# Optimization experiments

Measured on AMD Instinct MI355X. Metric: run time of the kernel, lower is better.

The kernel has to match this reference:

```python
import jax, jax.numpy as jnp
import numpy as np
from jax import lax

# LRN hyperparameters (from module __init__)
K = 2.0
KERNEL = 5
ALPHA = 1e-4
BETA = 0.75
PAD = KERNEL // 2


def setup_inputs() -> dict:
    key = jax.random.key(0)
    x = jax.random.normal(key, (16, 96, 224, 224), dtype=jnp.float32)
    return {"x": x}


def reference(x) -> jnp.ndarray:
    # Spatial local response norm: per-channel k x k box sum of squares
    # (equivalent to Unfold(kernel, pad=kernel//2) -> view -> square -> sum over window).
    sq = x * x
    ssq = lax.reduce_window(
        sq,
        jnp.float32(0.0),
        lax.add,
        window_dimensions=(1, 1, KERNEL, KERNEL),
        window_strides=(1, 1, 1, 1),
        padding=((0, 0), (0, 0), (PAD, PAD), (PAD, PAD)),
    )
    denom = (K + ALPHA * ssq) ** BETA
    return x / denom
```

## Files before the change

kernel.cpp:

```cpp
#include <hip/hip_runtime.h>


#define LRN_H 224
#define LRN_W 224
#define LRN_WQ 56
#define LRN_STRIPS 8
#define LRN_ROWS 28
#define LRN_PLANE (LRN_H * LRN_W)

__device__ __forceinline__ float4 lrn_zero4() { return make_float4(0.f, 0.f, 0.f, 0.f); }

__device__ __forceinline__ float4 lrn_rowsum(const float* __restrict__ px, int row, int col, int q) {
    if (row < 0 || row >= LRN_H) return lrn_zero4();
    const float* rp = px + row * LRN_W + col;
    float4 xc = *(const float4*)rp;
    float4 xl = (q > 0)          ? *(const float4*)(rp - 4) : lrn_zero4();
    float4 xr = (q < LRN_WQ - 1) ? *(const float4*)(rp + 4) : lrn_zero4();
    float a  = xl.z * xl.z;
    float b  = xl.w * xl.w;
    float c0 = xc.x * xc.x;
    float c1 = xc.y * xc.y;
    float c2 = xc.z * xc.z;
    float c3 = xc.w * xc.w;
    float d0 = xr.x * xr.x;
    float d1 = xr.y * xr.y;
    float t = c1 + c2;
    float4 r;
    r.x = a + b + c0 + t;
    r.y = b + c0 + t + c3;
    r.z = c0 + t + c3 + d0;
    r.w = t + c3 + d0 + d1;
    return r;
}

__global__ __launch_bounds__(256) void LocalResponseNorm_17420387352942_kernel(
        const float* __restrict__ x, float* __restrict__ out) {
    const int q = threadIdx.x;
    if (q >= LRN_WQ) return;
    const int job = blockIdx.x * 4 + threadIdx.y;
    const int plane = job >> 3;
    const int strip = job & 7;
    const float* px = x + (size_t)plane * LRN_PLANE;
    float* po = out + (size_t)plane * LRN_PLANE;
    const int s0 = strip * LRN_ROWS;
    const int col = q << 2;

    float4 r0 = lrn_rowsum(px, s0 - 2, col, q);
    float4 r1 = lrn_rowsum(px, s0 - 1, col, q);
    float4 r2 = lrn_rowsum(px, s0,     col, q);
    float4 r3 = lrn_rowsum(px, s0 + 1, col, q);

#pragma unroll
    for (int h = s0; h < s0 + LRN_ROWS; ++h) {
        float4 r4 = lrn_rowsum(px, h + 2, col, q);
        float4 s;
        s.x = r0.x + r1.x + r2.x + r3.x + r4.x;
        s.y = r0.y + r1.y + r2.y + r3.y + r4.y;
        s.z = r0.z + r1.z + r2.z + r3.z + r4.z;
        s.w = r0.w + r1.w + r2.w + r3.w + r4.w;

        float4 xv = *(const float4*)(px + h * LRN_W + col);
        float4 o;
        {
            float d = fmaf(1e-4f, s.x, 2.0f);
            float r = __builtin_amdgcn_rsqf(d);
            o.x = xv.x * r * __builtin_amdgcn_sqrtf(r);
        }
        {
            float d = fmaf(1e-4f, s.y, 2.0f);
            float r = __builtin_amdgcn_rsqf(d);
            o.y = xv.y * r * __builtin_amdgcn_sqrtf(r);
        }
        {
            float d = fmaf(1e-4f, s.z, 2.0f);
            float r = __builtin_amdgcn_rsqf(d);
            o.z = xv.z * r * __builtin_amdgcn_sqrtf(r);
        }
        {
            float d = fmaf(1e-4f, s.w, 2.0f);
            float r = __builtin_amdgcn_rsqf(d);
            o.w = xv.w * r * __builtin_amdgcn_sqrtf(r);
        }
        *(float4*)(po + h * LRN_W + col) = o;

        r0 = r1; r1 = r2; r2 = r3; r3 = r4;
    }
}

extern "C" void kernel_launch(void* const* d_in, const int* in_sizes, int n_in,
                              void* d_out, int out_size, void* d_ws, size_t ws_size,
                              hipStream_t stream) {
    const float* x = (const float*)d_in[0];
    float* out = (float*)d_out;
    dim3 block(64, 4, 1);
    dim3 grid(12288 / 4, 1, 1);
    LocalResponseNorm_17420387352942_kernel<<<grid, block, 0, stream>>>(x, out);
}
```

Before: 527.0 us.

## Pack threads densely, prefetch next row, reuse center loads, nontemporal stores

Threads are now packed densely, so no lanes idle (before, 8 of every 64 lanes exited). Strips are taller (56 rows), which cuts halo re-reads. Border handling uses clamped addresses and multiply masks instead of branches. Each row is loaded one iteration ahead for prefetch, and center values are kept in registers rather than re-read for the output. Stores are nontemporal and occupancy is hinted at 6 blocks. The cost is higher register pressure and fewer, longer-running jobs, which may reduce parallelism.

```diff
diff --git a/kernel.cpp b/kernel.cpp
--- a/kernel.cpp
+++ b/kernel.cpp
@@ -1,89 +1,115 @@
 #include <hip/hip_runtime.h>
 
+
+typedef float f4 __attribute__((ext_vector_type(4)));
 
 #define LRN_H 224
 #define LRN_W 224
 #define LRN_WQ 56
-#define LRN_STRIPS 8
-#define LRN_ROWS 28
+#define LRN_ROWS 56
+#define LRN_STRIPS 4
 #define LRN_PLANE (LRN_H * LRN_W)
 
-__device__ __forceinline__ float4 lrn_zero4() { return make_float4(0.f, 0.f, 0.f, 0.f); }
-
-__device__ __forceinline__ float4 lrn_rowsum(const float* __restrict__ px, int row, int col, int q) {
-    if (row < 0 || row >= LRN_H) return lrn_zero4();
-    const float* rp = px + row * LRN_W + col;
-    float4 xc = *(const float4*)rp;
-    float4 xl = (q > 0)          ? *(const float4*)(rp - 4) : lrn_zero4();
-    float4 xr = (q < LRN_WQ - 1) ? *(const float4*)(rp + 4) : lrn_zero4();
-    float a  = xl.z * xl.z;
-    float b  = xl.w * xl.w;
-    float c0 = xc.x * xc.x;
-    float c1 = xc.y * xc.y;
-    float c2 = xc.z * xc.z;
-    float c3 = xc.w * xc.w;
-    float d0 = xr.x * xr.x;
-    float d1 = xr.y * xr.y;
+__device__ __forceinline__ f4 lrn_hsum(f4 xl, f4 xc, f4 xr,
+                                       float mL, float mR, float mV) {
+    float a  = xl[2] * xl[2] * mL;
+    float b  = xl[3] * xl[3] * mL;
+    float c0 = xc[0] * xc[0];
+    float c1 = xc[1] * xc[1];
+    float c2 = xc[2] * xc[2];
+    float c3 = xc[3] * xc[3];
+    float d0 = xr[0] * xr[0] * mR;
+    float d1 = xr[1] * xr[1] * mR;
     float t = c1 + c2;
-    float4 r;
-    r.x = a + b + c0 + t;
-    r.y = b + c0 + t + c3;
-    r.z = c0 + t + c3 + d0;
-    r.w = t + c3 + d0 + d1;
+    f4 r;
+    r[0] = (a + b + c0 + t) * mV;
+    r[1] = (b + c0 + t + c3) * mV;
+    r[2] = (c0 + t + c3 + d0) * mV;
+    r[3] = (t + c3 + d0 + d1) * mV;
     return r;
 }
 
-__global__ __launch_bounds__(256) void LocalResponseNorm_17420387352942_kernel(
+__device__ __forceinline__ void lrn_load(const float* __restrict__ rp,
+                                         int offL, int offR,
+                                         f4& xl, f4& xc, f4& xr) {
+    xc = *(const f4*)rp;
+    xl = *(const f4*)(rp + offL);
+    xr = *(const f4*)(rp + offR);
+}
+
+__global__ __launch_bounds__(256, 6) void LocalResponseNorm_17420387352942_kernel(
         const float* __restrict__ x, float* __restrict__ out) {
-    const int q = threadIdx.x;
-    if (q >= LRN_WQ) return;
-    const int job = blockIdx.x * 4 + threadIdx.y;
-    const int plane = job >> 3;
-    const int strip = job & 7;
-    const float* px = x + (size_t)plane * LRN_PLANE;
-    float* po = out + (size_t)plane * LRN_PLANE;
-    const int s0 = strip * LRN_ROWS;
-    const int col = q << 2;
+    const int gid  = blockIdx.x * 256 + threadIdx.x;
+    const int job  = gid / LRN_WQ;
+    const int q    = gid - job * LRN_WQ;
+    const int plane = job >> 2;
+    const int strip = job & 3;
+    const int s0    = strip * LRN_ROWS;
 
-    float4 r0 = lrn_rowsum(px, s0 - 2, col, q);
-    float4 r1 = lrn_rowsum(px, s0 - 1, col, q);
-    float4 r2 = lrn_rowsum(px, s0,     col, q);
-    float4 r3 = lrn_rowsum(px, s0 + 1, col, q);
+    const float* __restrict__ px = x   + (size_t)plane * LRN_PLANE + (q << 2);
+    float* __restrict__       po = out + (size_t)plane * LRN_PLANE + (q << 2);
 
+    const float mL = (q > 0)           ? 1.0f : 0.0f;
+    const float mR = (q < LRN_WQ - 1)  ? 1.0f : 0.0f;
+    const int offL = (q > 0)           ? -4 : 0;
+    const int offR = (q < LRN_WQ - 1)  ?  4 : 0;
+
+    f4 Al, Ac, Ar;
+    f4 r0, r1, r2, r3;
+    f4 c0, c1;
+
+    {
+        int row = s0 - 2;
+        int rr  = max(row, 0);
+        float mV = (row >= 0) ? 1.0f : 0.0f;
+        lrn_load(px + rr * LRN_W, offL, offR, Al, Ac, Ar);
+        r0 = lrn_hsum(Al, Ac, Ar, mL, mR, mV);
+    }
+    {
+        int row = s0 - 1;
+        int rr  = max(row, 0);
+        float mV = (row >= 0) ? 1.0f : 0.0f;
+        lrn_load(px + rr * LRN_W, offL, offR, Al, Ac, Ar);
+        r1 = lrn_hsum(Al, Ac, Ar, mL, mR, mV);
+    }
+    {
+        lrn_load(px + s0 * LRN_W, offL, offR, Al, Ac, Ar);
+        r2 = lrn_hsum(Al, Ac, Ar, mL, mR, 1.0f);
+        c0 = Ac;
+    }
+    {
+        lrn_load(px + (s0 + 1) * LRN_W, offL, offR, Al, Ac, Ar);
+        r3 = lrn_hsum(Al, Ac, Ar, mL, mR, 1.0f);
+        c1 = Ac;
+    }
+    lrn_load(px + (s0 + 2) * LRN_W, offL, offR, Al, Ac, Ar);
+
+#pragma unroll 2
+    for (int i = 0; i < LRN_ROWS; ++i) {
+        const int hrow = s0 + i;
+
+        const float mV = (hrow + 2 < LRN_H) ? 1.0f : 0.0f;
+        f4 r4 = lrn_hsum(Al, Ac, Ar, mL, mR, mV);
+        f4 c2 = Ac;
+
+        {
+            int rr = min(hrow + 3, LRN_H - 1);
+            lrn_load(px + rr * LRN_W, offL, offR, Al, Ac, Ar);
+        }
+
+        f4 s = r0 + r1 + r2 + r3 + r4;
+
+        f4 o;
 #pragma unroll
-    for (int h = s0; h < s0 + LRN_ROWS; ++h) {
-        float4 r4 = lrn_rowsum(px, h + 2, col, q);
-        float4 s;
-        s.x = r0.x + r1.x + r2.x + r3.x + r4.x;
-        s.y = r0.y + r1.y + r2.y + r3.y + r4.y;
-        s.z = r0.z + r1.z + r2.z + r3.z + r4.z;
-        s.w = r0.w + r1.w + r2.w + r3.w + r4.w;
-
-        float4 xv = *(const float4*)(px + h * LRN_W + col);
-        float4 o;
-        {
-            float d = fmaf(1e-4f, s.x, 2.0f);
-            float r = __builtin_amdgcn_rsqf(d);
-            o.x = xv.x * r * __builtin_amdgcn_sqrtf(r);
+        for (int j = 0; j < 4; ++j) {
+            float d  = fmaf(1e-4f, s[j], 2.0f);
+            float rs = __builtin_amdgcn_rsqf(d);
+            o[j] = c0[j] * rs * __builtin_amdgcn_sqrtf(rs);
         }
-        {
-            float d = fmaf(1e-4f, s.y, 2.0f);
-            float r = __builtin_amdgcn_rsqf(d);
-            o.y = xv.y * r * __builtin_amdgcn_sqrtf(r);
-        }
-        {
-            float d = fmaf(1e-4f, s.z, 2.0f);
-            float r = __builtin_amdgcn_rsqf(d);
-            o.z = xv.z * r * __builtin_amdgcn_sqrtf(r);
-        }
-        {
-            float d = fmaf(1e-4f, s.w, 2.0f);
-            float r = __builtin_amdgcn_rsqf(d);
-            o.w = xv.w * r * __builtin_amdgcn_sqrtf(r);
-        }
-        *(float4*)(po + h * LRN_W + col) = o;
+        __builtin_nontemporal_store(o, (f4*)(po + hrow * LRN_W));
 
         r0 = r1; r1 = r2; r2 = r3; r3 = r4;
+        c0 = c1; c1 = c2;
     }
 }
 
@@ -92,7 +118,7 @@
                               hipStream_t stream) {
     const float* x = (const float*)d_in[0];
     float* out = (float*)d_out;
-    dim3 block(64, 4, 1);
-    dim3 grid(12288 / 4, 1, 1);
+    dim3 block(256, 1, 1);
+    dim3 grid(1344, 1, 1);
     LocalResponseNorm_17420387352942_kernel<<<grid, block, 0, stream>>>(x, out);
 }
```

Measured after the change: 536.9 us. About the same (+1.9%).

## Share row neighbours via wave shuffles and prefetch rows in registers

Applied to the files above, without the earlier changes.

Each thread now loads only its own float4 per row and gets the neighbouring squared values from adjacent lanes with shuffles, instead of issuing three overlapping loads per row. A rotating three-row register prefetch queue and reuse of the centre row from registers remove the separate reload of x for the output. Output stores use nontemporal hints, and idle lanes stay alive (clamped) so the shuffles work, with edge rows handled by multiplicative masks. This adds extra register pressure and shuffle instructions to lower global load traffic and latency stalls.

```diff
diff --git a/kernel.cpp b/kernel.cpp
--- a/kernel.cpp
+++ b/kernel.cpp
@@ -1,89 +1,93 @@
 #include <hip/hip_runtime.h>
 
+
+typedef float f4 __attribute__((ext_vector_type(4)));
 
 #define LRN_H 224
 #define LRN_W 224
 #define LRN_WQ 56
-#define LRN_STRIPS 8
 #define LRN_ROWS 28
 #define LRN_PLANE (LRN_H * LRN_W)
 
-__device__ __forceinline__ float4 lrn_zero4() { return make_float4(0.f, 0.f, 0.f, 0.f); }
+__device__ __forceinline__ f4 lrn_ld(const float* __restrict__ p) {
+    return *(const f4*)p;
+}
 
-__device__ __forceinline__ float4 lrn_rowsum(const float* __restrict__ px, int row, int col, int q) {
-    if (row < 0 || row >= LRN_H) return lrn_zero4();
-    const float* rp = px + row * LRN_W + col;
-    float4 xc = *(const float4*)rp;
-    float4 xl = (q > 0)          ? *(const float4*)(rp - 4) : lrn_zero4();
-    float4 xr = (q < LRN_WQ - 1) ? *(const float4*)(rp + 4) : lrn_zero4();
-    float a  = xl.z * xl.z;
-    float b  = xl.w * xl.w;
-    float c0 = xc.x * xc.x;
-    float c1 = xc.y * xc.y;
-    float c2 = xc.z * xc.z;
-    float c3 = xc.w * xc.w;
-    float d0 = xr.x * xr.x;
-    float d1 = xr.y * xr.y;
-    float t = c1 + c2;
-    float4 r;
-    r.x = a + b + c0 + t;
-    r.y = b + c0 + t + c3;
-    r.z = c0 + t + c3 + d0;
-    r.w = t + c3 + d0 + d1;
+__device__ __forceinline__ f4 lrn_rowsum_sh(f4 xc, bool okL, bool okR, float mV) {
+    f4 sq = xc * xc;
+    float a  = __shfl_up(sq[2], 1);
+    float b  = __shfl_up(sq[3], 1);
+    float d0 = __shfl_down(sq[0], 1);
+    float d1 = __shfl_down(sq[1], 1);
+    a  = okL ? a  : 0.0f;
+    b  = okL ? b  : 0.0f;
+    d0 = okR ? d0 : 0.0f;
+    d1 = okR ? d1 : 0.0f;
+    float t = sq[1] + sq[2];
+    f4 r;
+    r[0] = (a + b + sq[0] + t) * mV;
+    r[1] = (b + sq[0] + t + sq[3]) * mV;
+    r[2] = (sq[0] + t + sq[3] + d0) * mV;
+    r[3] = (t + sq[3] + d0 + d1) * mV;
     return r;
 }
 
 __global__ __launch_bounds__(256) void LocalResponseNorm_17420387352942_kernel(
         const float* __restrict__ x, float* __restrict__ out) {
-    const int q = threadIdx.x;
-    if (q >= LRN_WQ) return;
+    const int q   = threadIdx.x;
+    const int qe  = min(q, LRN_WQ - 1);
     const int job = blockIdx.x * 4 + threadIdx.y;
     const int plane = job >> 3;
     const int strip = job & 7;
-    const float* px = x + (size_t)plane * LRN_PLANE;
-    float* po = out + (size_t)plane * LRN_PLANE;
-    const int s0 = strip * LRN_ROWS;
-    const int col = q << 2;
+    const int s0    = strip * LRN_ROWS;
 
-    float4 r0 = lrn_rowsum(px, s0 - 2, col, q);
-    float4 r1 = lrn_rowsum(px, s0 - 1, col, q);
-    float4 r2 = lrn_rowsum(px, s0,     col, q);
-    float4 r3 = lrn_rowsum(px, s0 + 1, col, q);
+    const float* __restrict__ px = x   + (size_t)plane * LRN_PLANE + (qe << 2);
+    float* __restrict__       po = out + (size_t)plane * LRN_PLANE + (qe << 2);
+
+    const bool okL = (qe > 0);
+    const bool okR = (qe < LRN_WQ - 1);
+    const bool wr  = (q < LRN_WQ);
+
+    f4 x0 = lrn_ld(px + max(s0 - 2, 0) * LRN_W);
+    f4 x1 = lrn_ld(px + max(s0 - 1, 0) * LRN_W);
+    f4 x2 = lrn_ld(px + s0 * LRN_W);
+    f4 x3 = lrn_ld(px + (s0 + 1) * LRN_W);
+    f4 r0 = lrn_rowsum_sh(x0, okL, okR, (s0 - 2 >= 0) ? 1.0f : 0.0f);
+    f4 r1 = lrn_rowsum_sh(x1, okL, okR, (s0 - 1 >= 0) ? 1.0f : 0.0f);
+    f4 r2 = lrn_rowsum_sh(x2, okL, okR, 1.0f);
+    f4 r3 = lrn_rowsum_sh(x3, okL, okR, 1.0f);
+    f4 c0 = x2, c1 = x3;
+
+    f4 A0 = lrn_ld(px + min(s0 + 2, LRN_H - 1) * LRN_W);
+    f4 A1 = lrn_ld(px + min(s0 + 3, LRN_H - 1) * LRN_W);
+    f4 A2 = lrn_ld(px + min(s0 + 4, LRN_H - 1) * LRN_W);
 
 #pragma unroll
-    for (int h = s0; h < s0 + LRN_ROWS; ++h) {
-        float4 r4 = lrn_rowsum(px, h + 2, col, q);
-        float4 s;
-        s.x = r0.x + r1.x + r2.x + r3.x + r4.x;
-        s.y = r0.y + r1.y + r2.y + r3.y + r4.y;
-        s.z = r0.z + r1.z + r2.z + r3.z + r4.z;
-        s.w = r0.w + r1.w + r2.w + r3.w + r4.w;
+    for (int i = 0; i < LRN_ROWS; ++i) {
+        const int h = s0 + i;
 
-        float4 xv = *(const float4*)(px + h * LRN_W + col);
-        float4 o;
+        f4 cur = (i % 3 == 0) ? A0 : (i % 3 == 1) ? A1 : A2;
+        const float mV = (h + 2 < LRN_H) ? 1.0f : 0.0f;
+        f4 r4 = lrn_rowsum_sh(cur, okL, okR, mV);
+
         {
-            float d = fmaf(1e-4f, s.x, 2.0f);
-            float r = __builtin_amdgcn_rsqf(d);
-            o.x = xv.x * r * __builtin_amdgcn_sqrtf(r);
+            f4 nxt = lrn_ld(px + min(h + 5, LRN_H - 1) * LRN_W);
+            if (i % 3 == 0) A0 = nxt; else if (i % 3 == 1) A1 = nxt; else A2 = nxt;
         }
-        {
-            float d = fmaf(1e-4f, s.y, 2.0f);
-            float r = __builtin_amdgcn_rsqf(d);
-            o.y = xv.y * r * __builtin_amdgcn_sqrtf(r);
+
+        f4 s = r0 + r1 + r2 + r3 + r4;
+
+        f4 o;
+#pragma unroll
+        for (int j = 0; j < 4; ++j) {
+            float d  = fmaf(1e-4f, s[j], 2.0f);
+            float rs = __builtin_amdgcn_rsqf(d);
+            o[j] = c0[j] * rs * __builtin_amdgcn_sqrtf(rs);
         }
-        {
-            float d = fmaf(1e-4f, s.z, 2.0f);
-            float r = __builtin_amdgcn_rsqf(d);
-            o.z = xv.z * r * __builtin_amdgcn_sqrtf(r);
-        }
-        {
-            float d = fmaf(1e-4f, s.w, 2.0f);
-            float r = __builtin_amdgcn_rsqf(d);
-            o.w = xv.w * r * __builtin_amdgcn_sqrtf(r);
-        }
-        *(float4*)(po + h * LRN_W + col) = o;
+        if (wr) __builtin_nontemporal_store(o, (f4*)(po + h * LRN_W));
 
         r0 = r1; r1 = r2; r2 = r3; r3 = r4;
+        c0 = c1; c1 = cur;
     }
 }
 
@@ -93,6 +97,6 @@
     const float* x = (const float*)d_in[0];
     float* out = (float*)d_out;
     dim3 block(64, 4, 1);
-    dim3 grid(12288 / 4, 1, 1);
+    dim3 grid(3072, 1, 1);
     LocalResponseNorm_17420387352942_kernel<<<grid, block, 0, stream>>>(x, out);
 }
```

New measurement: 516.9 us. About the same (-1.9%).
